# Optimization experiments

Measured on AMD Instinct MI355X. Metric: run time of the kernel, lower is better.

Reference implementation:

```python
import jax, jax.numpy as jnp
import numpy as np

N_ITEMS = 50000
N_USERS = 20000
N_NODES = N_ITEMS + N_USERS
D = 128
N_REL = 3
NNZ = 800000
K_LAYERS = 2
B, S, L = 256, 4, 50


def setup_inputs() -> dict:
    key = jax.random.key(0)
    ks = iter(jax.random.split(key, 40))
    stdv = float(1.0 / np.sqrt(D))

    def uni(shape):
        return jax.random.uniform(next(ks), shape, jnp.float32, -stdv, stdv)

    id_emb = (jax.random.normal(next(ks), (N_ITEMS, D), jnp.float32) * 0.1).at[0].set(0.0)  # padding_idx=0
    user_emb = jax.random.normal(next(ks), (N_USERS, D), jnp.float32) * 0.1
    inp = dict(
        id_emb=id_emb, user_emb=user_emb,
        lin_r_w=uni((K_LAYERS, N_REL, D, D)),
        upi_w=uni((K_LAYERS, D, D)), upi_b=uni((K_LAYERS, D)),
        upu_w=uni((K_LAYERS, D, D)), upu_b=uni((K_LAYERS, D)),
        w_ih=uni((3 * D, 2 * D)), w_hh=uni((3 * D, D)),
        b_ih=uni((3 * D,)), b_hh=uni((3 * D,)),
        b_iah=uni((D,)), b_oah=uni((D,)),
        ei_w=uni((D, D)), ei_b=uni((D,)),
        eo_w=uni((D, D)), eo_b=uni((D,)),
        q1_w=uni((D, D)), q2_w=uni((D, D)), att_w=uni((D,)),
        fuse_w=uni((D, 2 * D)), fuse_b=uni((D,)),
    )
    # global heterogeneous graph: COO per relation over item+user nodes
    inp['rel_rows'] = jax.random.randint(next(ks), (N_REL, NNZ), 0, N_NODES, dtype=jnp.int32)
    inp['rel_cols'] = jax.random.randint(next(ks), (N_REL, NNZ), 0, N_NODES, dtype=jnp.int32)
    inp['rel_vals'] = jax.random.uniform(next(ks), (N_REL, NNZ), jnp.float32) * 0.1
    # session batch: every session has length in [2, L]
    lens = jax.random.randint(next(ks), (B, S), 2, L + 1)
    raw = jax.random.randint(next(ks), (B, S, L), 1, N_ITEMS)
    inp['ids'] = (raw * (jnp.arange(L)[None, None, :] < lens[:, :, None])).astype(jnp.int32)
    inp['uid'] = jax.random.randint(next(ks), (B,), 0, N_USERS, dtype=jnp.int32)
    inp['u_type'] = jax.random.randint(next(ks), (B,), 0, 3).astype(jnp.float32)
    return inp


def _hgnn(h_item, h_user, rel_rows, rel_cols, rel_vals, lin_r_w, upi_w, upi_b, upu_w, upu_b):
    Ni = h_item.shape[0]
    N = Ni + h_user.shape[0]
    for k in range(lin_r_w.shape[0]):
        h_all = jnp.concatenate([h_item, h_user], 0)
        msg = jnp.zeros_like(h_all)
        for r in range(rel_rows.shape[0]):
            Wh = h_all @ lin_r_w[k, r].T  # per-relation linear
            msg = msg + jax.ops.segment_sum(Wh[rel_cols[r]] * rel_vals[r][:, None],
                                            rel_rows[r], num_segments=N)  # sparse.mm
        h_item = jax.nn.relu((msg[:Ni] + h_item) @ upi_w[k].T + upi_b[k])
        h_user = jax.nn.relu((msg[Ni:] + h_user) @ upu_w[k].T + upu_b[k])
    return h_item, h_user


def reference(id_emb, user_emb, lin_r_w, upi_w, upi_b, upu_w, upu_b,
              w_ih, w_hh, b_ih, b_hh, b_iah, b_oah,
              ei_w, ei_b, eo_w, eo_b, q1_w, q2_w, att_w, fuse_w, fuse_b,
              rel_rows, rel_cols, rel_vals, ids, uid, u_type):
    Bb, Ss, Ll = ids.shape
    N = Ss * Bb
    ids_sb = jnp.transpose(ids, (1, 0, 2)).reshape(N, Ll)  # session-major, matches torch concat order
    lens = (ids_sb != 0).sum(-1)  # >= 2 by construction -> all sessions valid
    rows = jnp.arange(N)
    target = ids_sb[rows, lens - 1]
    Lp = Ll - 1
    m_in = jnp.arange(Lp)[None, :] < (lens - 1)[:, None]
    seq_in = ids_sb[:, :Lp] * m_in
    # session graph: consecutive-item edges; in-half sub-diagonal, out-half super-diagonal
    valid = (m_in[:, 1:] & m_in[:, :-1]).astype(jnp.float32)  # [N, Lp-1]
    i1 = jnp.arange(1, Lp)
    i0 = jnp.arange(Lp - 1)
    a_in = jnp.zeros((N, Lp, Lp), jnp.float32).at[:, i1, i0].set(valid)
    a_out = jnp.zeros((N, Lp, Lp), jnp.float32).at[:, i0, i1].set(valid)
    deg = jnp.clip(a_in.sum(-1), 1.0, None)[..., None]
    a_in = a_in / deg
    a_out = a_out / deg
    h = id_emb[seq_in]  # [N, Lp, D]
    # SessionGNN GRU-style cell (step=1)
    m_i = jnp.matmul(a_in, h @ ei_w.T + ei_b) + b_iah
    m_o = jnp.matmul(a_out, h @ eo_w.T + eo_b) + b_oah
    gi = jnp.concatenate([m_i, m_o], -1) @ w_ih.T + b_ih
    gh = h @ w_hh.T + b_hh
    i_r, i_i, i_n = jnp.split(gi, 3, -1)
    h_r, h_i, h_n = jnp.split(gh, 3, -1)
    rg = jax.nn.sigmoid(i_r + h_r)
    zg = jax.nn.sigmoid(i_i + h_i)
    ng = jnp.tanh(i_n + rg * h_n)
    h = ng + zg * (h - ng)
    # attention readout
    ht = h[rows, jnp.clip(lens - 2, 0, None)]
    alpha = jax.nn.sigmoid((ht @ q1_w.T)[:, None, :] + h @ q2_w.T) @ att_w  # [N, Lp]
    alpha = alpha * m_in.astype(jnp.float32)
    alpha = alpha / (alpha.sum(1, keepdims=True) + 1e-8)
    c_cur = jnp.einsum('nl,nld->nd', alpha, h)
    # global HGNN user context
    g_item, g_user = _hgnn(id_emb[:N_ITEMS], user_emb[:N_USERS], rel_rows, rel_cols,
                           rel_vals, lin_r_w, upi_w, upi_b, upu_w, upu_b)
    c_hist = g_user[jnp.tile(uid, Ss)]
    reps = jnp.concatenate([c_cur, c_hist], -1) @ fuse_w.T + fuse_b
    return reps, target, jnp.tile(u_type, Ss)
```

## Files before the change

### kernel.cpp

```cpp
#include <hip/hip_runtime.h>
#include <hip/hip_bf16.h>

typedef __hip_bfloat16 bf16;
typedef unsigned int uint32;
typedef __attribute__((ext_vector_type(8))) short short8;
typedef __attribute__((ext_vector_type(4))) float f32x4;
typedef __attribute__((ext_vector_type(2))) float f32x2;
typedef __attribute__((ext_vector_type(4))) uint32 u32x4;

#define N_ITEMS_C 50000
#define N_USERS_C 20000
#define N_NODES_C 70000
#define NNZ_C 800000
#define NSESS 1024
#define LP 49
#define NTOK (NSESS * LP)
#define NBK 137

__device__ __forceinline__ float bflo(uint32 u) { return __uint_as_float(u << 16); }
__device__ __forceinline__ float bfhi(uint32 u) { return __uint_as_float(u & 0xffff0000u); }
__device__ __forceinline__ float bfhi_fast(uint32 u) { return __uint_as_float(u); }
__device__ __forceinline__ uint32 packbf(float a, float b) {
    return (uint32)__bfloat16_as_ushort(__float2bfloat16(a)) |
           ((uint32)__bfloat16_as_ushort(__float2bfloat16(b)) << 16);
}

__global__ __launch_bounds__(256) void init_hist_kernel(
    const float4* __restrict__ idp, const float4* __restrict__ usp,
    uint32* __restrict__ hab, const int* __restrict__ rel_rows, int* __restrict__ bhist)
{
    __shared__ int hist[NBK];
    const int tid = threadIdx.x;
    if (blockIdx.x < 8750) {
        int i = blockIdx.x * 256 + tid;
        float4 w = (i < 1600000) ? idp[i] : usp[i - 1600000];
        uint2 o = make_uint2(packbf(w.x, w.y), packbf(w.z, w.w));
        *(uint2*)&hab[(size_t)i * 2] = o;
        return;
    }
    const int hb = blockIdx.x - 8750;
    const int r = hb / 196, xb = hb - r * 196;
    if (tid < NBK) hist[tid] = 0;
    __syncthreads();
    const int* rr = rel_rows + (size_t)r * NNZ_C;
#pragma unroll
    for (int i = 0; i < 16; ++i) {
        int e = xb * 4096 + i * 256 + tid;
        if (e < NNZ_C) atomicAdd(&hist[rr[e] >> 9], 1);
    }
    __syncthreads();
    if (tid < NBK && hist[tid]) atomicAdd(&bhist[r * NBK + tid], hist[tid]);
}

__global__ __launch_bounds__(256) void bucket_scan_kernel(
    const int* __restrict__ bhist, int* __restrict__ bbase)
{
    __shared__ int s[256];
    const int tid = threadIdx.x;
    for (int r = 0; r < 3; ++r) {
        s[tid] = (tid < NBK) ? bhist[r * NBK + tid] : 0;
        __syncthreads();
        for (int d = 1; d < 256; d <<= 1) {
            int t = (tid >= d) ? s[tid - d] : 0;
            __syncthreads();
            s[tid] += t;
            __syncthreads();
        }
        if (tid < NBK) bbase[r * (NBK + 1) + tid + 1] = s[tid];
        if (tid == 0) bbase[r * (NBK + 1)] = 0;
        __syncthreads();
    }
}

__global__ __launch_bounds__(256) void bucket_scatter_kernel(
    const int* __restrict__ rel_rows, const int* __restrict__ rel_cols,
    const float* __restrict__ rel_vals, const int* __restrict__ bbase,
    int* __restrict__ cursor, int2* __restrict__ tmp)
{
    __shared__ int hist[NBK], gbase[NBK], cur2[NBK];
    const int r = blockIdx.y, tid = threadIdx.x;
    if (tid < NBK) { hist[tid] = 0; cur2[tid] = 0; }
    __syncthreads();
    const int* rr = rel_rows + (size_t)r * NNZ_C;
    const int* rc = rel_cols + (size_t)r * NNZ_C;
    const float* rv = rel_vals + (size_t)r * NNZ_C;
    int rows[16];
#pragma unroll
    for (int i = 0; i < 16; ++i) {
        int e = blockIdx.x * 4096 + i * 256 + tid;
        rows[i] = (e < NNZ_C) ? rr[e] : -1;
        if (rows[i] >= 0) atomicAdd(&hist[rows[i] >> 9], 1);
    }
    __syncthreads();
    if (tid < NBK)
        gbase[tid] = bbase[r * (NBK + 1) + tid] +
                     (hist[tid] ? atomicAdd(&cursor[r * NBK + tid], hist[tid]) : 0);
    __syncthreads();
    int2* tp = tmp + (size_t)r * NNZ_C;
#pragma unroll
    for (int i = 0; i < 16; ++i) {
        int e = blockIdx.x * 4096 + i * 256 + tid;
        if (rows[i] >= 0) {
            int bk = rows[i] >> 9;
            int rank = atomicAdd(&cur2[bk], 1);
            uint32 fb = __float_as_uint(rv[e]);
            uint32 pk = (uint32)rc[e] | (((fb >> 16) & 0x7FFFu) << 17);
            tp[gbase[bk] + rank] = make_int2((int)pk, rows[i]);
        }
    }
}

__global__ __launch_bounds__(256) void bucket_refine_kernel(
    const int2* __restrict__ tmp, const int* __restrict__ bbase,
    int* __restrict__ offs, uint32* __restrict__ edges)
{
    __shared__ int cnt[512], offsL[512], cur[512];
    __shared__ uint32 outb[6656];
    const int b = blockIdx.x, r = blockIdx.y, tid = threadIdx.x;
    const int lane = tid & 63, wid = tid >> 6;
    const int row0 = b << 9;
    const int e0 = bbase[r * (NBK + 1) + b];
    const int e1 = bbase[r * (NBK + 1) + b + 1];
    cnt[tid] = 0; cnt[256 + tid] = 0; cur[tid] = 0; cur[256 + tid] = 0;
    __syncthreads();
    const int2* tp = tmp + (size_t)r * NNZ_C;
    for (int e = e0 + tid; e < e1; e += 256)
        atomicAdd(&cnt[tp[e].y - row0], 1);
    __syncthreads();
    if (wid == 0) {
        int carry = 0;
        for (int c = 0; c < 8; ++c) {
            int x = cnt[c * 64 + lane];
            int inc = x;
#pragma unroll
            for (int d = 1; d < 64; d <<= 1) {
                int y = __shfl_up(inc, d, 64);
                if (lane >= d) inc += y;
            }
            offsL[c * 64 + lane] = inc - x + carry;
            carry += __shfl(inc, 63, 64);
        }
    }
    __syncthreads();
    for (int i = tid; i < 512; i += 256) {
        int row = row0 + i;
        if (row < 70001) offs[(size_t)r * 70001 + row] = e0 + offsL[i];
    }
    for (int e = e0 + tid; e < e1; e += 256) {
        int2 E = tp[e];
        int lr_ = E.y - row0;
        int slot = offsL[lr_] + atomicAdd(&cur[lr_], 1);
        if (slot < 6656) outb[slot] = (uint32)E.x;
    }
    __syncthreads();
    uint32* eo = edges + (size_t)r * NNZ_C + e0;
    for (int i = tid; i < e1 - e0; i += 256) eo[i] = outb[i];
}

__global__ __launch_bounds__(256) void gather_kernel(
    const uint32* __restrict__ hab, const uint32* __restrict__ edges,
    const int* __restrict__ offs, uint32* __restrict__ T)
{
    const int row = blockIdx.x * 4 + (threadIdx.x >> 6);
    const int lane = threadIdx.x & 63;
    const int grp = lane >> 4;
    const int ql  = lane & 15;
    const char* __restrict__ habB = (const char*)hab + ql * 16;
    f32x2 acc[3][4];
#pragma unroll
    for (int r = 0; r < 3; ++r)
#pragma unroll
        for (int j = 0; j < 4; ++j) acc[r][j] = (f32x2){0.f, 0.f};
#pragma unroll
    for (int r = 0; r < 3; ++r) {
        const uint32* __restrict__ ed = edges + (size_t)r * NNZ_C;
        const int* __restrict__ of = offs + (size_t)r * 70001;
        const int e0 = of[row], e1 = of[row + 1];
        if (e0 >= e1) continue;
        const uint32 span = (uint32)(e1 - e0);
        const int s0 = e0 & ~3;
        for (int eb = s0; eb < e1; eb += 16) {
            const int base = eb + grp * 4;
            uint4 E4 = *(const uint4*)&ed[base];
            uint32 Ej0 = ((uint32)(base + 0 - e0) < span) ? E4.x : 0u;
            uint32 Ej1 = ((uint32)(base + 1 - e0) < span) ? E4.y : 0u;
            uint32 Ej2 = ((uint32)(base + 2 - e0) < span) ? E4.z : 0u;
            uint32 Ej3 = ((uint32)(base + 3 - e0) < span) ? E4.w : 0u;
            uint4 u0 = *(const uint4*)(habB + ((Ej0 & 0x1FFFFu) << 8));
            uint4 u1 = *(const uint4*)(habB + ((Ej1 & 0x1FFFFu) << 8));
            uint4 u2 = *(const uint4*)(habB + ((Ej2 & 0x1FFFFu) << 8));
            uint4 u3 = *(const uint4*)(habB + ((Ej3 & 0x1FFFFu) << 8));
            float v0 = __uint_as_float((Ej0 >> 1) & 0x7FFF0000u);
            float v1 = __uint_as_float((Ej1 >> 1) & 0x7FFF0000u);
            float v2 = __uint_as_float((Ej2 >> 1) & 0x7FFF0000u);
            float v3 = __uint_as_float((Ej3 >> 1) & 0x7FFF0000u);
            f32x2 vv;
            vv = (f32x2){v0, v0};
            acc[r][0] += vv * (f32x2){bflo(u0.x), bfhi_fast(u0.x)};
            acc[r][1] += vv * (f32x2){bflo(u0.y), bfhi_fast(u0.y)};
            acc[r][2] += vv * (f32x2){bflo(u0.z), bfhi_fast(u0.z)};
            acc[r][3] += vv * (f32x2){bflo(u0.w), bfhi_fast(u0.w)};
            vv = (f32x2){v1, v1};
            acc[r][0] += vv * (f32x2){bflo(u1.x), bfhi_fast(u1.x)};
            acc[r][1] += vv * (f32x2){bflo(u1.y), bfhi_fast(u1.y)};
            acc[r][2] += vv * (f32x2){bflo(u1.z), bfhi_fast(u1.z)};
            acc[r][3] += vv * (f32x2){bflo(u1.w), bfhi_fast(u1.w)};
            vv = (f32x2){v2, v2};
            acc[r][0] += vv * (f32x2){bflo(u2.x), bfhi_fast(u2.x)};
            acc[r][1] += vv * (f32x2){bflo(u2.y), bfhi_fast(u2.y)};
            acc[r][2] += vv * (f32x2){bflo(u2.z), bfhi_fast(u2.z)};
            acc[r][3] += vv * (f32x2){bflo(u2.w), bfhi_fast(u2.w)};
            vv = (f32x2){v3, v3};
            acc[r][0] += vv * (f32x2){bflo(u3.x), bfhi_fast(u3.x)};
            acc[r][1] += vv * (f32x2){bflo(u3.y), bfhi_fast(u3.y)};
            acc[r][2] += vv * (f32x2){bflo(u3.z), bfhi_fast(u3.z)};
            acc[r][3] += vv * (f32x2){bflo(u3.w), bfhi_fast(u3.w)};
        }
    }
    float* af = (float*)acc;
#pragma unroll
    for (int off = 16; off < 64; off <<= 1)
#pragma unroll
        for (int j = 0; j < 24; ++j) af[j] += __shfl_xor(af[j], off, 64);
    if (grp == 0) {
#pragma unroll
        for (int r = 0; r < 3; ++r) {
            u32x4 o;
            o.x = packbf(acc[r][0].x, acc[r][0].y);
            o.y = packbf(acc[r][1].x, acc[r][1].y);
            o.z = packbf(acc[r][2].x, acc[r][2].y);
            o.w = packbf(acc[r][3].x, acc[r][3].y);
            __builtin_nontemporal_store(o, (u32x4*)&T[(size_t)row * 192 + r * 64 + ql * 4]);
        }
    }
}

__global__ __launch_bounds__(256, 3) void wprep_kernel(
    const float* __restrict__ upi_w, const float* __restrict__ upu_w,
    const float* __restrict__ lin_r_w, uint32* __restrict__ Wcat)
{
    __shared__ float As[128][65];
    __shared__ __align__(8) bf16 Ws[128][66];
    const int which = blockIdx.y, seg = which / 3, r = which % 3;
    const int k = blockIdx.z;
    const float* U  = (seg == 0 ? upi_w : upu_w) + (size_t)k * 16384;
    const float* Wr = lin_r_w + (size_t)(k * 3 + r) * 16384;
    uint32* out = Wcat + (size_t)(k * 2 + seg) * 32768;
    const int tid = threadIdx.x;
    const int row0 = blockIdx.x * 64;
#pragma unroll
    for (int i = 0; i < 8; ++i) {
        int id = i * 256 + tid;
        int rr = id >> 5, c4 = (id & 31) << 2;
        float4 v = *(const float4*)&U[(size_t)(row0 + rr) * 128 + c4];
        As[c4][rr] = v.x; As[c4+1][rr] = v.y; As[c4+2][rr] = v.z; As[c4+3][rr] = v.w;
    }
    const int m0 = (tid & 15) * 4;
    const int n0 = (tid >> 4) * 8;
    float acc[4][8];
#pragma unroll
    for (int i = 0; i < 4; ++i)
#pragma unroll
        for (int j = 0; j < 8; ++j) acc[i][j] = 0.f;
    for (int p = 0; p < 2; ++p) {
        if (p) __syncthreads();
        for (int i = 0; i < 32; ++i) {
            int id = i * 256 + tid;
            int c = id >> 6, kf = id & 63;
            Ws[c][kf] = __float2bfloat16(Wr[(size_t)(p * 64 + kf) * 128 + c]);
        }
        __syncthreads();
        for (int k2 = 0; k2 < 32; ++k2) {
            int kk = p * 64 + 2 * k2;
            float av0[4], av1[4];
#pragma unroll
            for (int i = 0; i < 4; ++i) { av0[i] = As[kk][m0 + i]; av1[i] = As[kk + 1][m0 + i]; }
#pragma unroll
            for (int j = 0; j < 8; ++j) {
                uint32 wp = *(const uint32*)&Ws[n0 + j][2 * k2];
                float w0 = bflo(wp), w1 = bfhi(wp);
#pragma unroll
                for (int i = 0; i < 4; ++i)
                    acc[i][j] = fmaf(av1[i], w1, fmaf(av0[i], w0, acc[i][j]));
            }
        }
    }
#pragma unroll
    for (int i = 0; i < 4; ++i) {
        int n = row0 + m0 + i;
#pragma unroll
        for (int j = 0; j < 8; j += 2)
            out[(size_t)n * 256 + (r * 128 + n0 + j) / 2] = packbf(acc[i][j], acc[i][j + 1]);
    }
}

__global__ __launch_bounds__(256) void upack_kernel(
    const float* __restrict__ upi_w, const float* __restrict__ upu_w,
    uint32* __restrict__ Wcat)
{
    int id = blockIdx.x * 256 + threadIdx.x;
    int k = id >> 14, rest = id & 16383;
    int seg = rest >> 13, p = rest & 8191;
    int n = p >> 6, j2 = (p & 63);
    const float* U = (seg ? upu_w : upi_w) + (size_t)k * 16384;
    float2 w = *(const float2*)&U[(size_t)n * 128 + j2 * 2];
    Wcat[(size_t)(k * 2 + seg) * 32768 + (size_t)n * 256 + 192 + j2] = packbf(w.x, w.y);
}

#define HGNN_ITEM_BLOCKS 391
__global__ __launch_bounds__(256) void hgnn_update_mfma_kernel(
    const bf16* __restrict__ T, uint32* __restrict__ hab,
    const bf16* __restrict__ Wcat, const float* __restrict__ upi_b,
    const float* __restrict__ upu_b, int k)
{
    const int tid = threadIdx.x;
    const int wv = tid >> 6, lane = tid & 63, quad = lane >> 4, lr = lane & 15;
    const int bid = blockIdx.x;
    const int seg = (bid >= HGNN_ITEM_BLOCKS) ? 1 : 0;
    const int row0 = seg ? N_ITEMS_C : 0;
    const int M = seg ? N_USERS_C : N_ITEMS_C;
    const int rbase = (seg ? bid - HGNN_ITEM_BLOCKS : bid) * 128;
    const bf16* __restrict__ Wc = Wcat + (size_t)(k * 2 + seg) * 65536;
    const float* __restrict__ bias = (seg ? upu_b : upi_b) + k * 128;
    const bf16* hb = (const bf16*)hab;
    f32x4 acc[8][2];
#pragma unroll
    for (int mt = 0; mt < 8; ++mt) { acc[mt][0] = (f32x4){0,0,0,0}; acc[mt][1] = (f32x4){0,0,0,0}; }
    int arow[8];
#pragma unroll
    for (int mt = 0; mt < 8; ++mt) {
        int rr = rbase + mt * 16 + lr;
        arow[mt] = row0 + (rr < M ? rr : M - 1);
    }
#pragma unroll
    for (int ks = 0; ks < 16; ++ks) {
        short8 b0 = *(const short8*)&Wc[(size_t)(wv * 32 + lr) * 512 + ks * 32 + quad * 8];
        short8 b1 = *(const short8*)&Wc[(size_t)(wv * 32 + 16 + lr) * 512 + ks * 32 + quad * 8];
#pragma unroll
        for (int mt = 0; mt < 8; ++mt) {
            short8 a;
            if (ks < 12) a = *(const short8*)&T[(size_t)arow[mt] * 384 + ks * 32 + quad * 8];
            else         a = *(const short8*)&hb[(size_t)arow[mt] * 128 + (ks - 12) * 32 + quad * 8];
            acc[mt][0] = __builtin_amdgcn_mfma_f32_16x16x32_bf16(a, b0, acc[mt][0], 0, 0, 0);
            acc[mt][1] = __builtin_amdgcn_mfma_f32_16x16x32_bf16(a, b1, acc[mt][1], 0, 0, 0);
        }
    }
    __syncthreads();
    unsigned short* hw = (unsigned short*)hab;
#pragma unroll
    for (int s = 0; s < 2; ++s) {
        int col = wv * 32 + s * 16 + lr;
        float bv = bias[col];
#pragma unroll
        for (int mt = 0; mt < 8; ++mt)
#pragma unroll
            for (int reg = 0; reg < 4; ++reg) {
                int rr = rbase + mt * 16 + quad * 4 + reg;
                if (rr < M) {
                    float v = fmaxf(acc[mt][s][reg] + bv, 0.f);
                    hw[(size_t)(row0 + rr) * 128 + col] = __bfloat16_as_ushort(__float2bfloat16(v));
                }
            }
    }
}

__global__ __launch_bounds__(256) void mfma_nt_kernel(
    const bf16* __restrict__ A, const int* __restrict__ rowmap,
    const bf16* __restrict__ W0, const float* __restrict__ b0,
    float* __restrict__ O0, int M)
{
    const int tid = threadIdx.x;
    const int wv = tid >> 6, lane = tid & 63, quad = lane >> 4, lr = lane & 15;
    const int rbase = blockIdx.x * 128;
    int arow[8];
#pragma unroll
    for (int mt = 0; mt < 8; ++mt) {
        int rr = rbase + mt * 16 + lr;
        rr = rr < M ? rr : M - 1;
        arow[mt] = rowmap ? rowmap[rr] : rr;
    }
    f32x4 acc0[8][2];
#pragma unroll
    for (int mt = 0; mt < 8; ++mt) { acc0[mt][0] = (f32x4){0,0,0,0}; acc0[mt][1] = (f32x4){0,0,0,0}; }
#pragma unroll
    for (int ks = 0; ks < 4; ++ks) {
        short8 b00 = *(const short8*)&W0[(size_t)(wv * 32 + lr) * 128 + ks * 32 + quad * 8];
        short8 b01 = *(const short8*)&W0[(size_t)(wv * 32 + 16 + lr) * 128 + ks * 32 + quad * 8];
#pragma unroll
        for (int mt = 0; mt < 8; ++mt) {
            short8 a = *(const short8*)&A[(size_t)arow[mt] * 128 + ks * 32 + quad * 8];
            acc0[mt][0] = __builtin_amdgcn_mfma_f32_16x16x32_bf16(a, b00, acc0[mt][0], 0, 0, 0);
            acc0[mt][1] = __builtin_amdgcn_mfma_f32_16x16x32_bf16(a, b01, acc0[mt][1], 0, 0, 0);
        }
    }
#pragma unroll
    for (int s = 0; s < 2; ++s) {
        int col = wv * 32 + s * 16 + lr;
        float bv0 = b0 ? b0[col] : 0.f;
#pragma unroll
        for (int mt = 0; mt < 8; ++mt)
#pragma unroll
            for (int reg = 0; reg < 4; ++reg) {
                int rr = rbase + mt * 16 + quad * 4 + reg;
                if (rr < M) O0[(size_t)rr * 128 + col] = acc0[mt][s][reg] + bv0;
            }
    }
}

__global__ __launch_bounds__(256) void misc_prep_kernel(
    const int* __restrict__ ids, const int* __restrict__ uid,
    const float* __restrict__ u_type, const float* __restrict__ id_emb,
    const uint32* __restrict__ hab,
    const float* __restrict__ w_ih, const float* __restrict__ w_hh,
    const float* __restrict__ ei_w, const float* __restrict__ eo_w,
    const float* __restrict__ q2_w, const float* __restrict__ q1_w,
    const float* __restrict__ fuse_w,
    int* __restrict__ lens, int* __restrict__ rowmap,
    float* __restrict__ out_target, float* __restrict__ out_utype,
    float* __restrict__ chist, uint32* __restrict__ wdst,
    uint32* __restrict__ hb)
{
    const int bid = blockIdx.x, tid = threadIdx.x;
    if (bid < 4) {
        int n = bid * 256 + tid;
        if (n >= NSESS) return;
        int b = n & 255, s = n >> 8;
        const int* row = ids + (size_t)(b * 4 + s) * 50;
        int len = 0;
#pragma unroll
        for (int l = 0; l < 50; ++l) len += (row[l] != 0) ? 1 : 0;
        lens[n] = len;
        rowmap[n] = n * LP + (len - 2);
        out_target[n] = (float)row[len - 1];
        out_utype[n] = u_type[b];
        return;
    }
    if (bid < 516) {
        int n = (bid - 4) * 2 + (tid >> 7);
        int d = tid & 127;
        uint32 u = hab[(size_t)(N_ITEMS_C + uid[n & 255]) * 64 + (d >> 1)];
        chist[(size_t)n * 128 + d] = (d & 1) ? bfhi(u) : bflo(u);
        return;
    }
    if (bid < 1060) {
        int id = (bid - 516) * 256 + tid;
        if (id >= 106496) {
            if (id >= 139264) return;
            int f = id - 106496;
            int kk = f >> 7, n = f & 127;
            ((float*)wdst)[id] = fuse_w[(size_t)n * 256 + kk];
            return;
        }
        const float* src; int off;
        if      (id <  49152) { src = w_ih; off = id; }
        else if (id <  73728) { src = w_hh; off = id - 49152; }
        else if (id <  81920) { src = ei_w; off = id - 73728; }
        else if (id <  90112) { src = eo_w; off = id - 81920; }
        else if (id <  98304) { src = q2_w; off = id - 90112; }
        else                  { src = q1_w; off = id - 98304; }
        float2 w = *(const float2*)&src[(size_t)off * 2];
        wdst[id] = packbf(w.x, w.y);
        return;
    }
    int g = (bid - 1060) * 4 + (tid >> 6);
    int d = tid & 63;
    int n = g / LP;
    int tt = g - n * LP;
    int b = n & 255, s = n >> 8;
    const int* row = ids + (size_t)(b * 4 + s) * 50;
    int v = (d < 50) ? row[d] : 0;
    unsigned long long bal = __ballot(v != 0);
    int len = __popcll(bal);
    int id0 = (tt < len - 1) ? row[tt] : 0;
    float2 e = *(const float2*)&id_emb[(size_t)id0 * 128 + d * 2];
    hb[(size_t)g * 64 + d] = packbf(e.x, e.y);
}

__global__ __launch_bounds__(256) void gru_fused_kernel(
    const uint32* __restrict__ hb,
    unsigned short* __restrict__ hb2,
    const bf16* __restrict__ Wi, const bf16* __restrict__ Wo,
    const bf16* __restrict__ wihb,
    const bf16* __restrict__ whhb,
    const float* __restrict__ ei_b, const float* __restrict__ eo_b,
    const float* __restrict__ b_iah, const float* __restrict__ b_oah,
    const float* __restrict__ b_ih, const float* __restrict__ b_hh,
    const int* __restrict__ lens)
{
    __shared__ __align__(16) bf16 Agi[32][264];
    const int tid = threadIdx.x;
    const int wv = tid >> 6;
    const int lane = tid & 63;
    const int quad = lane >> 4;
    const int lr = lane & 15;
    const int c0 = wv * 32;
    const int g0 = blockIdx.x * 32;
    const bf16* hbb = (const bf16*)hb;

    int arows[4];
#pragma unroll
    for (int t = 0; t < 4; ++t) {
        int r = g0 + (t - 1) * 16 + lr;
        arows[t] = (r < 0) ? r + NTOK : (r >= NTOK ? r - NTOK : r);
    }
    f32x4 aEi[3][2], aEo[3][2];
#pragma unroll
    for (int t = 0; t < 3; ++t) {
        aEi[t][0] = (f32x4){0,0,0,0}; aEi[t][1] = (f32x4){0,0,0,0};
        aEo[t][0] = (f32x4){0,0,0,0}; aEo[t][1] = (f32x4){0,0,0,0};
    }
#pragma unroll
    for (int ks = 0; ks < 4; ++ks) {
        short8 bi0 = *(const short8*)&Wi[(size_t)(wv * 32 + lr) * 128 + ks * 32 + quad * 8];
        short8 bi1 = *(const short8*)&Wi[(size_t)(wv * 32 + 16 + lr) * 128 + ks * 32 + quad * 8];
        short8 bo0 = *(const short8*)&Wo[(size_t)(wv * 32 + lr) * 128 + ks * 32 + quad * 8];
        short8 bo1 = *(const short8*)&Wo[(size_t)(wv * 32 + 16 + lr) * 128 + ks * 32 + quad * 8];
        short8 a[4];
#pragma unroll
        for (int t = 0; t < 4; ++t)
            a[t] = *(const short8*)&hbb[(size_t)arows[t] * 128 + ks * 32 + quad * 8];
#pragma unroll
        for (int t = 0; t < 3; ++t) {
            aEi[t][0] = __builtin_amdgcn_mfma_f32_16x16x32_bf16(a[t], bi0, aEi[t][0], 0, 0, 0);
            aEi[t][1] = __builtin_amdgcn_mfma_f32_16x16x32_bf16(a[t], bi1, aEi[t][1], 0, 0, 0);
            aEo[t][0] = __builtin_amdgcn_mfma_f32_16x16x32_bf16(a[t + 1], bo0, aEo[t][0], 0, 0, 0);
            aEo[t][1] = __builtin_amdgcn_mfma_f32_16x16x32_bf16(a[t + 1], bo1, aEo[t][1], 0, 0, 0);
        }
    }
#pragma unroll
    for (int s = 0; s < 2; ++s) {
        int col = c0 + s * 16 + lr;
        float bei = ei_b[col], beo = eo_b[col];
        float bia = b_iah[col], boa = b_oah[col];
#pragma unroll
        for (int t = 0; t < 3; ++t)
#pragma unroll
            for (int reg = 0; reg < 4; ++reg) {
                int src = g0 + (t - 1) * 16 + quad * 4 + reg;
                int ssrc = (src < 0) ? src + NTOK : (src >= NTOK ? src - NTOK : src);
                int d1 = ssrc + 1; if (d1 == NTOK) d1 = 0;
                int ld = d1 - g0;
                if ((unsigned)ld < 32u) {
                    int n1 = d1 / LP, t1 = d1 - n1 * LP, l1 = lens[n1];
                    float v = bia + ((t1 >= 1 && t1 < l1 - 1) ? aEi[t][s][reg] + bei : 0.f);
                    Agi[ld][col] = __float2bfloat16(v);
                }
                int src2 = g0 + t * 16 + quad * 4 + reg;
                int ssrc2 = (src2 >= NTOK) ? src2 - NTOK : src2;
                int d2 = (ssrc2 == 0) ? NTOK - 1 : ssrc2 - 1;
                int ld2 = d2 - g0;
                if ((unsigned)ld2 < 32u) {
                    int n2 = d2 / LP, t2 = d2 - n2 * LP, l2 = lens[n2];
                    float v = boa + ((t2 < l2 - 2) ? aEo[t][s][reg] + beo : 0.f);
                    Agi[ld2][128 + col] = __float2bfloat16(v);
                }
            }
    }
    __syncthreads();

    int arow[2];
#pragma unroll
    for (int mt = 0; mt < 2; ++mt) arow[mt] = g0 + mt * 16 + lr;
    f32x4 acc[2][2][4];
#pragma unroll
    for (int mt = 0; mt < 2; ++mt)
#pragma unroll
        for (int s = 0; s < 2; ++s)
#pragma unroll
            for (int j = 0; j < 4; ++j) acc[mt][s][j] = (f32x4){0.f, 0.f, 0.f, 0.f};

#pragma unroll 2
    for (int ks = 0; ks < 8; ++ks) {
        short8 bfr[2][3];
#pragma unroll
        for (int s = 0; s < 2; ++s)
#pragma unroll
            for (int gte = 0; gte < 3; ++gte) {
                int n0 = gte * 128 + c0 + s * 16 + lr;
                bfr[s][gte] = *(const short8*)&wihb[(size_t)n0 * 256 + ks * 32 + quad * 8];
            }
#pragma unroll
        for (int mt = 0; mt < 2; ++mt) {
            short8 a = *(const short8*)&Agi[mt * 16 + lr][ks * 32 + quad * 8];
#pragma unroll
            for (int s = 0; s < 2; ++s) {
                acc[mt][s][0] = __builtin_amdgcn_mfma_f32_16x16x32_bf16(a, bfr[s][0], acc[mt][s][0], 0, 0, 0);
                acc[mt][s][1] = __builtin_amdgcn_mfma_f32_16x16x32_bf16(a, bfr[s][1], acc[mt][s][1], 0, 0, 0);
                acc[mt][s][2] = __builtin_amdgcn_mfma_f32_16x16x32_bf16(a, bfr[s][2], acc[mt][s][2], 0, 0, 0);
            }
        }
    }
#pragma unroll 2
    for (int ks = 0; ks < 4; ++ks) {
        short8 bfr[2][3];
#pragma unroll
        for (int s = 0; s < 2; ++s)
#pragma unroll
            for (int gte = 0; gte < 3; ++gte) {
                int n0 = gte * 128 + c0 + s * 16 + lr;
                bfr[s][gte] = *(const short8*)&whhb[(size_t)n0 * 128 + ks * 32 + quad * 8];
            }
#pragma unroll
        for (int mt = 0; mt < 2; ++mt) {
            short8 a = *(const short8*)&hbb[(size_t)arow[mt] * 128 + ks * 32 + quad * 8];
#pragma unroll
            for (int s = 0; s < 2; ++s) {
                acc[mt][s][0] = __builtin_amdgcn_mfma_f32_16x16x32_bf16(a, bfr[s][0], acc[mt][s][0], 0, 0, 0);
                acc[mt][s][1] = __builtin_amdgcn_mfma_f32_16x16x32_bf16(a, bfr[s][1], acc[mt][s][1], 0, 0, 0);
                acc[mt][s][3] = __builtin_amdgcn_mfma_f32_16x16x32_bf16(a, bfr[s][2], acc[mt][s][3], 0, 0, 0);
            }
        }
    }

    const unsigned short* hold = (const unsigned short*)hb;
#pragma unroll
    for (int s = 0; s < 2; ++s) {
        int col = c0 + s * 16 + lr;
        float brz = b_ih[col] + b_hh[col];
        float bzz = b_ih[col + 128] + b_hh[col + 128];
        float bin = b_ih[col + 256];
        float bhn = b_hh[col + 256];
#pragma unroll
        for (int mt = 0; mt < 2; ++mt)
#pragma unroll
            for (int reg = 0; reg < 4; ++reg) {
                int row = g0 + mt * 16 + quad * 4 + reg;
                float rg = 1.f / (1.f + expf(-(acc[mt][s][0][reg] + brz)));
                float zg = 1.f / (1.f + expf(-(acc[mt][s][1][reg] + bzz)));
                float ng = tanhf(acc[mt][s][2][reg] + bin + rg * (acc[mt][s][3][reg] + bhn));
                size_t idx = (size_t)row * 128 + col;
                float ho = __uint_as_float((uint32)hold[idx] << 16);
                hb2[idx] = __bfloat16_as_ushort(__float2bfloat16(ng + zg * (ho - ng)));
            }
    }
}

__global__ __launch_bounds__(256) void q2alpha_kernel(
    const bf16* __restrict__ A,
    const bf16* __restrict__ W0,
    const float* __restrict__ q1h, const float* __restrict__ att_w,
    const int* __restrict__ lens, float* __restrict__ alG)
{
    __shared__ float red[4][128];
    const int tid = threadIdx.x;
    const int wv = tid >> 6, lane = tid & 63, quad = lane >> 4, lr = lane & 15;
    const int rbase = blockIdx.x * 128;
    f32x4 acc0[8][2];
#pragma unroll
    for (int mt = 0; mt < 8; ++mt) { acc0[mt][0] = (f32x4){0,0,0,0}; acc0[mt][1] = (f32x4){0,0,0,0}; }
#pragma unroll
    for (int ks = 0; ks < 4; ++ks) {
        short8 b00 = *(const short8*)&W0[(size_t)(wv * 32 + lr) * 128 + ks * 32 + quad * 8];
        short8 b01 = *(const short8*)&W0[(size_t)(wv * 32 + 16 + lr) * 128 + ks * 32 + quad * 8];
#pragma unroll
        for (int mt = 0; mt < 8; ++mt) {
            short8 a = *(const short8*)&A[(size_t)(rbase + mt * 16 + lr) * 128 + ks * 32 + quad * 8];
            acc0[mt][0] = __builtin_amdgcn_mfma_f32_16x16x32_bf16(a, b00, acc0[mt][0], 0, 0, 0);
            acc0[mt][1] = __builtin_amdgcn_mfma_f32_16x16x32_bf16(a, b01, acc0[mt][1], 0, 0, 0);
        }
    }
    const int colA = wv * 32 + lr, colB = colA + 16;
    const float awA = att_w[colA], awB = att_w[colB];
#pragma unroll
    for (int mt = 0; mt < 8; ++mt)
#pragma unroll
        for (int reg = 0; reg < 4; ++reg) {
            int row = rbase + mt * 16 + quad * 4 + reg;
            int n = row / LP;
            float q1A = q1h[(size_t)n * 128 + colA];
            float q1B = q1h[(size_t)n * 128 + colB];
            float p = awA / (1.f + expf(-(q1A + acc0[mt][0][reg])))
                    + awB / (1.f + expf(-(q1B + acc0[mt][1][reg])));
            p += __shfl_xor(p, 1, 64);
            p += __shfl_xor(p, 2, 64);
            p += __shfl_xor(p, 4, 64);
            p += __shfl_xor(p, 8, 64);
            if (lr == 0) red[wv][mt * 16 + quad * 4 + reg] = p;
        }
    __syncthreads();
    if (tid < 128) {
        int row = rbase + tid;
        int n = row / LP, t = row - n * LP;
        float s = red[0][tid] + red[1][tid] + red[2][tid] + red[3][tid];
        alG[row] = (t < lens[n] - 1) ? s : 0.f;
    }
}

__global__ __launch_bounds__(128) void attn_fuse_kernel(
    const float* __restrict__ alG, const unsigned short* __restrict__ hu,
    const float* __restrict__ chist, const int* __restrict__ lens,
    const float* __restrict__ ftwf, const float* __restrict__ fuse_b,
    float* __restrict__ out)
{
    __shared__ float al[64], cv[256];
    const int n = blockIdx.x, tid = threadIdx.x;
    if (tid < 64) al[tid] = (tid < LP) ? alG[(size_t)n * LP + tid] : 0.f;
    __syncthreads();
    const int len = lens[n];
    float ssum = 0.f;
    for (int t = 0; t < len - 1; ++t) ssum += al[t];
    float inv = 1.f / (ssum + 1e-8f);
    float c = 0.f;
    for (int t = 0; t < len - 1; ++t) {
        float hv = __uint_as_float((uint32)hu[(size_t)(n * LP + t) * 128 + tid] << 16);
        c += al[t] * inv * hv;
    }
    cv[tid] = c;
    cv[128 + tid] = chist[(size_t)n * 128 + tid];
    __syncthreads();
    float s = fuse_b[tid];
    for (int kk = 0; kk < 256; ++kk)
        s += cv[kk] * ftwf[(size_t)kk * 128 + tid];
    out[(size_t)n * 128 + tid] = s;
}

extern "C" void kernel_launch(void* const* d_in, const int* in_sizes, int n_in,
                              void* d_out, int out_size, void* d_ws, size_t ws_size,
                              hipStream_t stream)
{
    const float* id_emb   = (const float*)d_in[0];
    const float* user_emb = (const float*)d_in[1];
    const float* lin_r_w  = (const float*)d_in[2];
    const float* upi_w    = (const float*)d_in[3];
    const float* upi_b    = (const float*)d_in[4];
    const float* upu_w    = (const float*)d_in[5];
    const float* upu_b    = (const float*)d_in[6];
    const float* w_ih     = (const float*)d_in[7];
    const float* w_hh     = (const float*)d_in[8];
    const float* b_ih     = (const float*)d_in[9];
    const float* b_hh     = (const float*)d_in[10];
    const float* b_iah    = (const float*)d_in[11];
    const float* b_oah    = (const float*)d_in[12];
    const float* ei_w     = (const float*)d_in[13];
    const float* ei_b     = (const float*)d_in[14];
    const float* eo_w     = (const float*)d_in[15];
    const float* eo_b     = (const float*)d_in[16];
    const float* q1_w     = (const float*)d_in[17];
    const float* q2_w     = (const float*)d_in[18];
    const float* att_w    = (const float*)d_in[19];
    const float* fuse_w   = (const float*)d_in[20];
    const float* fuse_b   = (const float*)d_in[21];
    const int*  rel_rows  = (const int*)d_in[22];
    const int*  rel_cols  = (const int*)d_in[23];
    const float* rel_vals = (const float*)d_in[24];
    const int*  ids       = (const int*)d_in[25];
    const int*  uid       = (const int*)d_in[26];
    const float* u_type   = (const float*)d_in[27];
    float* out = (float*)d_out;

    uint32* W32    = (uint32*)d_ws;
    uint32* hab    = W32;
    uint32* T      = W32 + 4480000;
    uint32* edges  = W32 + 17920000;
    int2*   tmp    = (int2*)(W32 + 20320000);
    int*    offs   = (int*)(W32 + 25120000);
    int*    bhist  = (int*)(W32 + 25330004);
    int*    cursor = (int*)(W32 + 25330415);
    int*    bbase  = (int*)(W32 + 25330826);
    float*  q1h    = (float*)(W32 + 25396776);
    float*  chist  = (float*)(W32 + 25527848);
    int*    lens   = (int*)(W32 + 25658920);
    int*    rowmap = (int*)(W32 + 25659944);
    float*  alG    = (float*)(W32 + 25660968);
    uint32* Wcat   = W32 + 25711144;
    uint32* sess_hb = W32 + 20320000;
    unsigned short* hb2 = (unsigned short*)(W32 + 10902528);
    uint32* wpk     = W32 + 17920000;
    uint32* wihb = wpk;
    uint32* whhb = wpk + 49152;
    uint32* eiwb = wpk + 73728;
    uint32* eowb = wpk + 81920;
    uint32* q2wb = wpk + 90112;
    uint32* q1wb = wpk + 98304;
    float*  ftwf = (float*)(wpk + 106496);
    if (ws_size < (size_t)27144192 * 4 + 4096) return;

    hipMemsetAsync(bhist, 0, (size_t)822 * 4, stream);
    init_hist_kernel<<<9338, 256, 0, stream>>>((const float4*)id_emb, (const float4*)user_emb,
                                               hab, rel_rows, bhist);
    bucket_scan_kernel<<<1, 256, 0, stream>>>(bhist, bbase);
    bucket_scatter_kernel<<<dim3(196, 3), 256, 0, stream>>>(rel_rows, rel_cols, rel_vals,
                                                            bbase, cursor, tmp);
    bucket_refine_kernel<<<dim3(NBK, 3), 256, 0, stream>>>(tmp, bbase, offs, edges);

    wprep_kernel<<<dim3(2, 6, 2), 256, 0, stream>>>(upi_w, upu_w, lin_r_w, Wcat);
    upack_kernel<<<128, 256, 0, stream>>>(upi_w, upu_w, Wcat);

    for (int k = 0; k < 2; ++k) {
        gather_kernel<<<17500, 256, 0, stream>>>(hab, edges, offs, T);
        hgnn_update_mfma_kernel<<<548, 256, 0, stream>>>((const bf16*)T, hab,
            (const bf16*)Wcat, upi_b, upu_b, k);
    }

    misc_prep_kernel<<<13604, 256, 0, stream>>>(ids, uid, u_type, id_emb, hab,
        w_ih, w_hh, ei_w, eo_w, q2_w, q1_w, fuse_w,
        lens, rowmap, out + 131072, out + 132096, chist, wpk, sess_hb);
    gru_fused_kernel<<<1568, 256, 0, stream>>>(sess_hb, hb2,
        (const bf16*)eiwb, (const bf16*)eowb,
        (const bf16*)wihb, (const bf16*)whhb,
        ei_b, eo_b, b_iah, b_oah, b_ih, b_hh, lens);
    mfma_nt_kernel<<<8, 256, 0, stream>>>((const bf16*)hb2, rowmap,
        (const bf16*)q1wb, nullptr, q1h, NSESS);
    q2alpha_kernel<<<392, 256, 0, stream>>>((const bf16*)hb2, (const bf16*)q2wb,
        q1h, att_w, lens, alG);
    attn_fuse_kernel<<<NSESS, 128, 0, stream>>>(alG, (const unsigned short*)hb2,
        chist, lens, ftwf, fuse_b, out);
}
```

Before: 710.1 us.

## Fuse small prep kernels, compute q1 inside q2alpha, precompute per-token masks

Merges the weight-packing upack kernel into wprep, removes the standalone q1 GEMM kernel by computing the per-session q1 projection inside q2alpha through extra MFMAs and shared memory, and moves the chist gather into attn_fuse. misc_prep now writes a per-token byte mask so the GRU and alpha kernels read one byte instead of doing integer division and a lens lookup. The aim is fewer launches and less index arithmetic. In exchange, each q2alpha block recomputes a 16-session q1 tile, which is redundant work across blocks.

```diff
diff --git a/kernel.cpp b/kernel.cpp
--- a/kernel.cpp
+++ b/kernel.cpp
@@ -235,19 +235,30 @@
     }
 }
 
-__global__ __launch_bounds__(256, 3) void wprep_kernel(
+__global__ __launch_bounds__(256, 3) void wprep_upack_kernel(
     const float* __restrict__ upi_w, const float* __restrict__ upu_w,
     const float* __restrict__ lin_r_w, uint32* __restrict__ Wcat)
 {
     __shared__ float As[128][65];
     __shared__ __align__(8) bf16 Ws[128][66];
-    const int which = blockIdx.y, seg = which / 3, r = which % 3;
-    const int k = blockIdx.z;
+    const int tid = threadIdx.x;
+    if (blockIdx.x >= 24) {
+        int id = (blockIdx.x - 24) * 256 + tid;
+        int k = id >> 14, rest = id & 16383;
+        int seg = rest >> 13, p = rest & 8191;
+        int n = p >> 6, j2 = (p & 63);
+        const float* U = (seg ? upu_w : upi_w) + (size_t)k * 16384;
+        float2 w = *(const float2*)&U[(size_t)n * 128 + j2 * 2];
+        Wcat[(size_t)(k * 2 + seg) * 32768 + (size_t)n * 256 + 192 + j2] = packbf(w.x, w.y);
+        return;
+    }
+    const int xb = blockIdx.x & 1, rest = blockIdx.x >> 1;
+    const int which = rest % 6, k = rest / 6;
+    const int seg = which / 3, r = which % 3;
     const float* U  = (seg == 0 ? upi_w : upu_w) + (size_t)k * 16384;
     const float* Wr = lin_r_w + (size_t)(k * 3 + r) * 16384;
     uint32* out = Wcat + (size_t)(k * 2 + seg) * 32768;
-    const int tid = threadIdx.x;
-    const int row0 = blockIdx.x * 64;
+    const int row0 = xb * 64;
 #pragma unroll
     for (int i = 0; i < 8; ++i) {
         int id = i * 256 + tid;
@@ -292,19 +303,6 @@
         for (int j = 0; j < 8; j += 2)
             out[(size_t)n * 256 + (r * 128 + n0 + j) / 2] = packbf(acc[i][j], acc[i][j + 1]);
     }
-}
-
-__global__ __launch_bounds__(256) void upack_kernel(
-    const float* __restrict__ upi_w, const float* __restrict__ upu_w,
-    uint32* __restrict__ Wcat)
-{
-    int id = blockIdx.x * 256 + threadIdx.x;
-    int k = id >> 14, rest = id & 16383;
-    int seg = rest >> 13, p = rest & 8191;
-    int n = p >> 6, j2 = (p & 63);
-    const float* U = (seg ? upu_w : upi_w) + (size_t)k * 16384;
-    float2 w = *(const float2*)&U[(size_t)n * 128 + j2 * 2];
-    Wcat[(size_t)(k * 2 + seg) * 32768 + (size_t)n * 256 + 192 + j2] = packbf(w.x, w.y);
 }
 
 #define HGNN_ITEM_BLOCKS 391
@@ -364,61 +362,17 @@
     }
 }
 
-__global__ __launch_bounds__(256) void mfma_nt_kernel(
-    const bf16* __restrict__ A, const int* __restrict__ rowmap,
-    const bf16* __restrict__ W0, const float* __restrict__ b0,
-    float* __restrict__ O0, int M)
-{
-    const int tid = threadIdx.x;
-    const int wv = tid >> 6, lane = tid & 63, quad = lane >> 4, lr = lane & 15;
-    const int rbase = blockIdx.x * 128;
-    int arow[8];
-#pragma unroll
-    for (int mt = 0; mt < 8; ++mt) {
-        int rr = rbase + mt * 16 + lr;
-        rr = rr < M ? rr : M - 1;
-        arow[mt] = rowmap ? rowmap[rr] : rr;
-    }
-    f32x4 acc0[8][2];
-#pragma unroll
-    for (int mt = 0; mt < 8; ++mt) { acc0[mt][0] = (f32x4){0,0,0,0}; acc0[mt][1] = (f32x4){0,0,0,0}; }
-#pragma unroll
-    for (int ks = 0; ks < 4; ++ks) {
-        short8 b00 = *(const short8*)&W0[(size_t)(wv * 32 + lr) * 128 + ks * 32 + quad * 8];
-        short8 b01 = *(const short8*)&W0[(size_t)(wv * 32 + 16 + lr) * 128 + ks * 32 + quad * 8];
-#pragma unroll
-        for (int mt = 0; mt < 8; ++mt) {
-            short8 a = *(const short8*)&A[(size_t)arow[mt] * 128 + ks * 32 + quad * 8];
-            acc0[mt][0] = __builtin_amdgcn_mfma_f32_16x16x32_bf16(a, b00, acc0[mt][0], 0, 0, 0);
-            acc0[mt][1] = __builtin_amdgcn_mfma_f32_16x16x32_bf16(a, b01, acc0[mt][1], 0, 0, 0);
-        }
-    }
-#pragma unroll
-    for (int s = 0; s < 2; ++s) {
-        int col = wv * 32 + s * 16 + lr;
-        float bv0 = b0 ? b0[col] : 0.f;
-#pragma unroll
-        for (int mt = 0; mt < 8; ++mt)
-#pragma unroll
-            for (int reg = 0; reg < 4; ++reg) {
-                int rr = rbase + mt * 16 + quad * 4 + reg;
-                if (rr < M) O0[(size_t)rr * 128 + col] = acc0[mt][s][reg] + bv0;
-            }
-    }
-}
-
 __global__ __launch_bounds__(256) void misc_prep_kernel(
-    const int* __restrict__ ids, const int* __restrict__ uid,
-    const float* __restrict__ u_type, const float* __restrict__ id_emb,
-    const uint32* __restrict__ hab,
+    const int* __restrict__ ids, const float* __restrict__ u_type,
+    const float* __restrict__ id_emb,
     const float* __restrict__ w_ih, const float* __restrict__ w_hh,
     const float* __restrict__ ei_w, const float* __restrict__ eo_w,
     const float* __restrict__ q2_w, const float* __restrict__ q1_w,
     const float* __restrict__ fuse_w,
     int* __restrict__ lens, int* __restrict__ rowmap,
     float* __restrict__ out_target, float* __restrict__ out_utype,
-    float* __restrict__ chist, uint32* __restrict__ wdst,
-    uint32* __restrict__ hb)
+    uint32* __restrict__ wdst, uint32* __restrict__ hb,
+    unsigned char* __restrict__ maskG)
 {
     const int bid = blockIdx.x, tid = threadIdx.x;
     if (bid < 4) {
@@ -435,15 +389,8 @@
         out_utype[n] = u_type[b];
         return;
     }
-    if (bid < 516) {
-        int n = (bid - 4) * 2 + (tid >> 7);
-        int d = tid & 127;
-        uint32 u = hab[(size_t)(N_ITEMS_C + uid[n & 255]) * 64 + (d >> 1)];
-        chist[(size_t)n * 128 + d] = (d & 1) ? bfhi(u) : bflo(u);
-        return;
-    }
-    if (bid < 1060) {
-        int id = (bid - 516) * 256 + tid;
+    if (bid < 548) {
+        int id = (bid - 4) * 256 + tid;
         if (id >= 106496) {
             if (id >= 139264) return;
             int f = id - 106496;
@@ -462,7 +409,7 @@
         wdst[id] = packbf(w.x, w.y);
         return;
     }
-    int g = (bid - 1060) * 4 + (tid >> 6);
+    int g = (bid - 548) * 4 + (tid >> 6);
     int d = tid & 63;
     int n = g / LP;
     int tt = g - n * LP;
@@ -474,6 +421,13 @@
     int id0 = (tt < len - 1) ? row[tt] : 0;
     float2 e = *(const float2*)&id_emb[(size_t)id0 * 128 + d * 2];
     hb[(size_t)g * 64 + d] = packbf(e.x, e.y);
+    if (d == 0) {
+        unsigned char m = 0;
+        if (tt >= 1 && tt < len - 1) m |= 1;
+        if (tt < len - 2) m |= 2;
+        if (tt < len - 1) m |= 4;
+        maskG[g] = m;
+    }
 }
 
 __global__ __launch_bounds__(256) void gru_fused_kernel(
@@ -485,7 +439,7 @@
     const float* __restrict__ ei_b, const float* __restrict__ eo_b,
     const float* __restrict__ b_iah, const float* __restrict__ b_oah,
     const float* __restrict__ b_ih, const float* __restrict__ b_hh,
-    const int* __restrict__ lens)
+    const unsigned char* __restrict__ maskG)
 {
     __shared__ __align__(16) bf16 Agi[32][264];
     const int tid = threadIdx.x;
@@ -541,8 +495,7 @@
                 int d1 = ssrc + 1; if (d1 == NTOK) d1 = 0;
                 int ld = d1 - g0;
                 if ((unsigned)ld < 32u) {
-                    int n1 = d1 / LP, t1 = d1 - n1 * LP, l1 = lens[n1];
-                    float v = bia + ((t1 >= 1 && t1 < l1 - 1) ? aEi[t][s][reg] + bei : 0.f);
+                    float v = bia + ((maskG[d1] & 1) ? aEi[t][s][reg] + bei : 0.f);
                     Agi[ld][col] = __float2bfloat16(v);
                 }
                 int src2 = g0 + t * 16 + quad * 4 + reg;
@@ -550,8 +503,7 @@
                 int d2 = (ssrc2 == 0) ? NTOK - 1 : ssrc2 - 1;
                 int ld2 = d2 - g0;
                 if ((unsigned)ld2 < 32u) {
-                    int n2 = d2 / LP, t2 = d2 - n2 * LP, l2 = lens[n2];
-                    float v = boa + ((t2 < l2 - 2) ? aEo[t][s][reg] + beo : 0.f);
+                    float v = boa + ((maskG[d2] & 2) ? aEo[t][s][reg] + beo : 0.f);
                     Agi[ld2][128 + col] = __float2bfloat16(v);
                 }
             }
@@ -638,13 +590,20 @@
 __global__ __launch_bounds__(256) void q2alpha_kernel(
     const bf16* __restrict__ A,
     const bf16* __restrict__ W0,
-    const float* __restrict__ q1h, const float* __restrict__ att_w,
-    const int* __restrict__ lens, float* __restrict__ alG)
+    const bf16* __restrict__ Wq1,
+    const int* __restrict__ rowmap, const float* __restrict__ att_w,
+    const unsigned char* __restrict__ maskG, float* __restrict__ alG)
 {
     __shared__ float red[4][128];
+    __shared__ float q1s[16][128];
     const int tid = threadIdx.x;
     const int wv = tid >> 6, lane = tid & 63, quad = lane >> 4, lr = lane & 15;
     const int rbase = blockIdx.x * 128;
+    const int ns0 = rbase / LP;
+    int ns = ns0 + lr; if (ns > NSESS - 1) ns = NSESS - 1;
+    const int qrow = rowmap[ns];
+    f32x4 q1a[2];
+    q1a[0] = (f32x4){0,0,0,0}; q1a[1] = (f32x4){0,0,0,0};
     f32x4 acc0[8][2];
 #pragma unroll
     for (int mt = 0; mt < 8; ++mt) { acc0[mt][0] = (f32x4){0,0,0,0}; acc0[mt][1] = (f32x4){0,0,0,0}; }
@@ -652,6 +611,11 @@
     for (int ks = 0; ks < 4; ++ks) {
         short8 b00 = *(const short8*)&W0[(size_t)(wv * 32 + lr) * 128 + ks * 32 + quad * 8];
         short8 b01 = *(const short8*)&W0[(size_t)(wv * 32 + 16 + lr) * 128 + ks * 32 + quad * 8];
+        short8 bq0 = *(const short8*)&Wq1[(size_t)(wv * 32 + lr) * 128 + ks * 32 + quad * 8];
+        short8 bq1 = *(const short8*)&Wq1[(size_t)(wv * 32 + 16 + lr) * 128 + ks * 32 + quad * 8];
+        short8 aq = *(const short8*)&A[(size_t)qrow * 128 + ks * 32 + quad * 8];
+        q1a[0] = __builtin_amdgcn_mfma_f32_16x16x32_bf16(aq, bq0, q1a[0], 0, 0, 0);
+        q1a[1] = __builtin_amdgcn_mfma_f32_16x16x32_bf16(aq, bq1, q1a[1], 0, 0, 0);
 #pragma unroll
         for (int mt = 0; mt < 8; ++mt) {
             short8 a = *(const short8*)&A[(size_t)(rbase + mt * 16 + lr) * 128 + ks * 32 + quad * 8];
@@ -659,6 +623,12 @@
             acc0[mt][1] = __builtin_amdgcn_mfma_f32_16x16x32_bf16(a, b01, acc0[mt][1], 0, 0, 0);
         }
     }
+#pragma unroll
+    for (int s = 0; s < 2; ++s)
+#pragma unroll
+        for (int reg = 0; reg < 4; ++reg)
+            q1s[quad * 4 + reg][wv * 32 + s * 16 + lr] = q1a[s][reg];
+    __syncthreads();
     const int colA = wv * 32 + lr, colB = colA + 16;
     const float awA = att_w[colA], awB = att_w[colB];
 #pragma unroll
@@ -667,8 +637,8 @@
         for (int reg = 0; reg < 4; ++reg) {
             int row = rbase + mt * 16 + quad * 4 + reg;
             int n = row / LP;
-            float q1A = q1h[(size_t)n * 128 + colA];
-            float q1B = q1h[(size_t)n * 128 + colB];
+            float q1A = q1s[n - ns0][colA];
+            float q1B = q1s[n - ns0][colB];
             float p = awA / (1.f + expf(-(q1A + acc0[mt][0][reg])))
                     + awB / (1.f + expf(-(q1B + acc0[mt][1][reg])));
             p += __shfl_xor(p, 1, 64);
@@ -680,15 +650,15 @@
     __syncthreads();
     if (tid < 128) {
         int row = rbase + tid;
-        int n = row / LP, t = row - n * LP;
         float s = red[0][tid] + red[1][tid] + red[2][tid] + red[3][tid];
-        alG[row] = (t < lens[n] - 1) ? s : 0.f;
+        alG[row] = (maskG[row] & 4) ? s : 0.f;
     }
 }
 
 __global__ __launch_bounds__(128) void attn_fuse_kernel(
     const float* __restrict__ alG, const unsigned short* __restrict__ hu,
-    const float* __restrict__ chist, const int* __restrict__ lens,
+    const uint32* __restrict__ hab, const int* __restrict__ uid,
+    const int* __restrict__ lens,
     const float* __restrict__ ftwf, const float* __restrict__ fuse_b,
     float* __restrict__ out)
 {
@@ -706,7 +676,8 @@
         c += al[t] * inv * hv;
     }
     cv[tid] = c;
-    cv[128 + tid] = chist[(size_t)n * 128 + tid];
+    uint32 u = hab[(size_t)(N_ITEMS_C + uid[n & 255]) * 64 + (tid >> 1)];
+    cv[128 + tid] = (tid & 1) ? bfhi(u) : bflo(u);
     __syncthreads();
     float s = fuse_b[tid];
     for (int kk = 0; kk < 256; ++kk)
@@ -757,12 +728,11 @@
     int*    bhist  = (int*)(W32 + 25330004);
     int*    cursor = (int*)(W32 + 25330415);
     int*    bbase  = (int*)(W32 + 25330826);
-    float*  q1h    = (float*)(W32 + 25396776);
-    float*  chist  = (float*)(W32 + 25527848);
     int*    lens   = (int*)(W32 + 25658920);
     int*    rowmap = (int*)(W32 + 25659944);
     float*  alG    = (float*)(W32 + 25660968);
     uint32* Wcat   = W32 + 25711144;
+    unsigned char* maskG = (unsigned char*)(W32 + 25842216);
     uint32* sess_hb = W32 + 20320000;
     unsigned short* hb2 = (unsigned short*)(W32 + 10902528);
     uint32* wpk     = W32 + 17920000;
@@ -783,8 +753,7 @@
                                                             bbase, cursor, tmp);
     bucket_refine_kernel<<<dim3(NBK, 3), 256, 0, stream>>>(tmp, bbase, offs, edges);
 
-    wprep_kernel<<<dim3(2, 6, 2), 256, 0, stream>>>(upi_w, upu_w, lin_r_w, Wcat);
-    upack_kernel<<<128, 256, 0, stream>>>(upi_w, upu_w, Wcat);
+    wprep_upack_kernel<<<152, 256, 0, stream>>>(upi_w, upu_w, lin_r_w, Wcat);
 
     for (int k = 0; k < 2; ++k) {
         gather_kernel<<<17500, 256, 0, stream>>>(hab, edges, offs, T);
@@ -792,17 +761,15 @@
             (const bf16*)Wcat, upi_b, upu_b, k);
     }
 
-    misc_prep_kernel<<<13604, 256, 0, stream>>>(ids, uid, u_type, id_emb, hab,
+    misc_prep_kernel<<<13092, 256, 0, stream>>>(ids, u_type, id_emb,
         w_ih, w_hh, ei_w, eo_w, q2_w, q1_w, fuse_w,
-        lens, rowmap, out + 131072, out + 132096, chist, wpk, sess_hb);
+        lens, rowmap, out + 131072, out + 132096, wpk, sess_hb, maskG);
     gru_fused_kernel<<<1568, 256, 0, stream>>>(sess_hb, hb2,
         (const bf16*)eiwb, (const bf16*)eowb,
         (const bf16*)wihb, (const bf16*)whhb,
-        ei_b, eo_b, b_iah, b_oah, b_ih, b_hh, lens);
-    mfma_nt_kernel<<<8, 256, 0, stream>>>((const bf16*)hb2, rowmap,
-        (const bf16*)q1wb, nullptr, q1h, NSESS);
+        ei_b, eo_b, b_iah, b_oah, b_ih, b_hh, maskG);
     q2alpha_kernel<<<392, 256, 0, stream>>>((const bf16*)hb2, (const bf16*)q2wb,
-        q1h, att_w, lens, alG);
+        (const bf16*)q1wb, rowmap, att_w, maskG, alG);
     attn_fuse_kernel<<<NSESS, 128, 0, stream>>>(alG, (const unsigned short*)hb2,
-        chist, lens, ftwf, fuse_b, out);
-}
+        hab, uid, lens, ftwf, fuse_b, out);
+}
```

Result: no change. 696.3 us (-2.0%).
